# Kernel optimization log

Measured on AMD Instinct MI355X. Metric: run time of the kernel, lower is better.

## Reference

```python
import jax, jax.numpy as jnp
import numpy as np
from jax import lax

PADDING_L = 30  # causal: kernel_size - 1


def setup_inputs() -> dict:
    key = jax.random.key(0)
    k1, k2 = jax.random.split(key)
    T, B, C = 4096, 8, 1024
    H, K = 16, 31
    x = jax.random.normal(k1, (T, B, C), dtype=jnp.float32)
    weight = jax.random.normal(k2, (H, K), dtype=jnp.float32)
    return {"x": x, "weight": weight}


def reference(x, weight):
    # x: [T, B, C]; weight: [H, K]
    T, B, C = x.shape
    H, K = weight.shape
    R = C // H  # channels per head share the same kernel
    # weight_softmax=True: normalize kernel taps per head
    w = jax.nn.softmax(weight, axis=-1)            # [H, K]
    wc = jnp.repeat(w, R, axis=0)[:, None, :]      # [C, 1, K] depthwise kernel
    xb = jnp.transpose(x, (1, 2, 0))               # [B, C, T]
    # lightconv_cuda: out[b,c,t] = sum_k w[h(c),k] * x_pad[b,c,t+k],
    # left pad = padding_l, right pad = K-1-padding_l (cross-correlation)
    out = lax.conv_general_dilated(
        xb, wc,
        window_strides=(1,),
        padding=[(PADDING_L, K - 1 - PADDING_L)],
        feature_group_count=C,
        dimension_numbers=("NCH", "OIH", "NCH"),
    )                                              # [B, C, T]
    return jnp.transpose(out, (2, 0, 1))           # [T, B, C]
```

## Files before the change

### kernel.cpp

```cpp
#include <hip/hip_runtime.h>
#include <math.h>

#define T_DIM 4096
#define B_DIM 8
#define C_DIM 1024
#define H_DIM 16
#define K_DIM 31
#define PAD_L 30
#define TILE_T 64
#define BLOCK 256

__global__ __launch_bounds__(BLOCK) void lightconv_kernel(
    const float* __restrict__ x,
    const float* __restrict__ w,
    float* __restrict__ out)
{
    __shared__ float s_taps[4][K_DIM];

    const int tid    = threadIdx.x;
    const int colBlk = blockIdx.x;
    const int tBlk   = blockIdx.y;
    const int cc     = colBlk * BLOCK + tid;
    const int t0     = tBlk * TILE_T;

    if (tid < 4) {
        const int c0 = (colBlk * BLOCK) % C_DIM;
        const int h  = (c0 >> 6) + tid;
        const float* wr = w + h * K_DIM;
        float m = -1e30f;
        #pragma unroll
        for (int k = 0; k < K_DIM; ++k) m = fmaxf(m, wr[k]);
        float s = 0.0f;
        #pragma unroll
        for (int k = 0; k < K_DIM; ++k) {
            float e = __expf(wr[k] - m);
            s_taps[tid][k] = e;
            s += e;
        }
        const float inv = 1.0f / s;
        #pragma unroll
        for (int k = 0; k < K_DIM; ++k) s_taps[tid][k] *= inv;
    }
    __syncthreads();

    float taps[K_DIM];
    const int hl = tid >> 6;
    #pragma unroll
    for (int k = 0; k < K_DIM; ++k) taps[k] = s_taps[hl][k];

    const long stride = (long)B_DIM * C_DIM;
    float xv[TILE_T + PAD_L];
    #pragma unroll
    for (int j = 0; j < TILE_T + PAD_L; ++j) {
        const int t = t0 + j - PAD_L;
        xv[j] = (t >= 0) ? x[(long)t * stride + cc] : 0.0f;
    }

    #pragma unroll
    for (int i = 0; i < TILE_T; ++i) {
        float acc = 0.0f;
        #pragma unroll
        for (int k = 0; k < K_DIM; ++k)
            acc = fmaf(taps[k], xv[i + k], acc);
        out[(long)(t0 + i) * stride + cc] = acc;
    }
}

extern "C" void kernel_launch(void* const* d_in, const int* in_sizes, int n_in,
                              void* d_out, int out_size, void* d_ws, size_t ws_size,
                              hipStream_t stream) {
    const float* x = (const float*)d_in[0];
    const float* w = (const float*)d_in[1];
    float* out = (float*)d_out;

    dim3 grid((B_DIM * C_DIM) / BLOCK, T_DIM / TILE_T);
    lightconv_kernel<<<grid, BLOCK, 0, stream>>>(x, w, out);
}
```

Measured before the change: 234.8 us.

## Halve time tile, scalarize taps, split accumulators, hoist boundary check

Shrinks the time tile from 64 to 32 and asks for two blocks per CU, cutting the per-thread register window to raise occupancy. Taps are broadcast through readfirstlane so they can sit in scalar registers. The FMA chain is split into four independent accumulators to expose ILP, and the causal-padding check is moved out of the load loop. The halo reload fraction rises with the smaller tile: 62 rows are loaded per 32 outputs instead of 94 per 64, and the summation order changes slightly.

After: 236.5 us. No clear change (+0.7%).

```diff
diff --git a/kernel.cpp b/kernel.cpp
--- a/kernel.cpp
+++ b/kernel.cpp
@@ -7,10 +7,11 @@
 #define H_DIM 16
 #define K_DIM 31
 #define PAD_L 30
-#define TILE_T 64
+#define TILE_T 32
+#define WIN (TILE_T + PAD_L)
 #define BLOCK 256
 
-__global__ __launch_bounds__(BLOCK) void lightconv_kernel(
+__global__ __launch_bounds__(BLOCK, 2) void lightconv_kernel(
     const float* __restrict__ x,
     const float* __restrict__ w,
     float* __restrict__ out)
@@ -43,26 +44,40 @@
     }
     __syncthreads();
 
+    const int hl = tid >> 6;
     float taps[K_DIM];
-    const int hl = tid >> 6;
     #pragma unroll
-    for (int k = 0; k < K_DIM; ++k) taps[k] = s_taps[hl][k];
+    for (int k = 0; k < K_DIM; ++k) {
+        taps[k] = __int_as_float(
+            __builtin_amdgcn_readfirstlane(__float_as_int(s_taps[hl][k])));
+    }
 
     const long stride = (long)B_DIM * C_DIM;
-    float xv[TILE_T + PAD_L];
-    #pragma unroll
-    for (int j = 0; j < TILE_T + PAD_L; ++j) {
-        const int t = t0 + j - PAD_L;
-        xv[j] = (t >= 0) ? x[(long)t * stride + cc] : 0.0f;
+
+    float xv[WIN];
+    const float* px = x + (long)(t0 - PAD_L) * stride + cc;
+    if (t0 >= PAD_L) {
+        #pragma unroll
+        for (int j = 0; j < WIN; ++j) xv[j] = px[(long)j * stride];
+    } else {
+        #pragma unroll
+        for (int j = 0; j < WIN; ++j)
+            xv[j] = (j >= PAD_L) ? px[(long)j * stride] : 0.0f;
     }
 
+    float* po = out + (long)t0 * stride + cc;
     #pragma unroll
     for (int i = 0; i < TILE_T; ++i) {
-        float acc = 0.0f;
+        float a0 = 0.0f, a1 = 0.0f, a2 = 0.0f, a3 = 0.0f;
         #pragma unroll
-        for (int k = 0; k < K_DIM; ++k)
-            acc = fmaf(taps[k], xv[i + k], acc);
-        out[(long)(t0 + i) * stride + cc] = acc;
+        for (int k = 0; k < 8; ++k)  a0 = fmaf(taps[k],      xv[i + k],      a0);
+        #pragma unroll
+        for (int k = 0; k < 8; ++k)  a1 = fmaf(taps[8 + k],  xv[i + 8 + k],  a1);
+        #pragma unroll
+        for (int k = 0; k < 8; ++k)  a2 = fmaf(taps[16 + k], xv[i + 16 + k], a2);
+        #pragma unroll
+        for (int k = 0; k < 7; ++k)  a3 = fmaf(taps[24 + k], xv[i + 24 + k], a3);
+        po[(long)i * stride] = (a0 + a1) + (a2 + a3);
     }
 }
 
```
